# Kernel tuning notes

Hardware: AMD Instinct MI355X
Metric: run time of the kernel (lower is better)

Reference implementation:

```python
import jax, jax.numpy as jnp
import numpy as np

N_HEADS = 16
D_HEAD = 64
N_ROTATE = 32
ROPE_BASE = 10000.0
MAX_LEN = 2048  # round_up_to_multiple_of_256(keep count); static for jit
BATCH, SEQ = 2, 4096


def setup_inputs() -> dict:
    key = jax.random.key(0)
    kq, kk, kv = jax.random.split(key, 3)
    q = jax.random.normal(kq, (BATCH, N_HEADS, MAX_LEN, D_HEAD), jnp.float32)
    k = jax.random.normal(kk, (BATCH, N_HEADS, SEQ, D_HEAD), jnp.float32)
    v = jax.random.normal(kv, (BATCH, N_HEADS, SEQ, D_HEAD), jnp.float32)
    # causal full mask [batch, seq, seq] and full position ids [batch, seq]
    mask_full = jnp.broadcast_to(jnp.tril(jnp.ones((SEQ, SEQ), bool)), (BATCH, SEQ, SEQ))
    pos_full = jnp.broadcast_to(jnp.arange(SEQ, dtype=jnp.int32), (BATCH, SEQ))
    # skip_mask: exactly MAX_LEN kept tokens per row (random positions)
    rng = np.random.default_rng(0)
    sm = np.zeros((BATCH, SEQ), dtype=bool)
    for i in range(BATCH):
        sm[i, rng.permutation(SEQ)[:MAX_LEN]] = True
    return {"q": q, "k": k, "v": v, "mask_full": mask_full,
            "pos_full": pos_full, "skip_mask": jnp.asarray(sm)}


def _rope_rotate(x, pos):
    # x: [b, h, L, n_rotate], pos: [b, L]
    half = N_ROTATE // 2
    inv_freq = 1.0 / (ROPE_BASE ** (jnp.arange(0, N_ROTATE, 2, dtype=jnp.float32) / N_ROTATE))
    freqs = pos.astype(jnp.float32)[..., None] * inv_freq          # [b, L, half]
    emb = jnp.concatenate([freqs, freqs], axis=-1)[:, None]        # [b, 1, L, n_rotate]
    cos, sin = jnp.cos(emb), jnp.sin(emb)
    x1, x2 = x[..., :half], x[..., half:]
    rot = jnp.concatenate([-x2, x1], axis=-1)                      # rotate_half
    return x * cos + rot * sin


def reference(q, k, v, mask_full, pos_full, skip_mask):
    b, S = skip_mask.shape
    lengths = skip_mask.sum(axis=1)
    # vectorized _trim_attention_mask: stable argsort compacts kept indices to the front
    order = jnp.argsort(jnp.where(skip_mask, 0, 1), axis=1, stable=True)
    idx = order[:, :MAX_LEN]                                       # [b, max_len]
    brow = jnp.arange(b)[:, None]
    mask_trim = mask_full[brow, idx]                               # [b, max_len, S]
    pos_trim = pos_full[brow, idx]                                 # [b, max_len]
    valid = jnp.arange(MAX_LEN)[None, :] < lengths[:, None]
    mask_trim = mask_trim & valid[..., None]
    pos_trim = jnp.where(valid, pos_trim, 0)

    # partial RoPE on first n_rotate channels
    rq = _rope_rotate(q[..., :N_ROTATE], pos_trim)
    rk = _rope_rotate(k[..., :N_ROTATE], pos_full)
    q = jnp.concatenate([rq, q[..., N_ROTATE:]], axis=-1)
    k = jnp.concatenate([rk, k[..., N_ROTATE:]], axis=-1)

    # masked SDPA (bool mask broadcast over heads)
    scale = 1.0 / jnp.sqrt(jnp.float32(D_HEAD))
    scores = jnp.einsum('bhqd,bhkd->bhqk', q, k) * scale
    scores = jnp.where(mask_trim[:, None], scores, jnp.finfo(scores.dtype).min)
    attn = jax.nn.softmax(scores, axis=-1)
    return jnp.einsum('bhqk,bhkd->bhqd', attn, v)
```

## Files before the change

kernel.cpp:

```cpp
#include <hip/hip_runtime.h>
#include <math.h>

#define BB 2
#define HH 16
#define QQ 2048
#define SS 4096
#define DD 64
#define NRH 16
#define NQT 32

typedef unsigned short u16;
typedef unsigned int   u32;
typedef short bhalf8 __attribute__((ext_vector_type(8)));
typedef float f32x4  __attribute__((ext_vector_type(4)));

typedef __attribute__((address_space(1))) const u32 gu32;
typedef __attribute__((address_space(3))) u32 lu32;

#if __has_builtin(__builtin_amdgcn_exp2f)
#define EXP2(x) __builtin_amdgcn_exp2f(x)
#else
#define EXP2(x) exp2f(x)
#endif

union Frag16 { uint4 u; bhalf8 v; u16 s[8]; uint2 d[2]; };

__device__ __forceinline__ u16 f2bf(float f) {
  union { float f; u32 u; } c; c.f = f;
  return (u16)((c.u + 0x7FFFu + ((c.u >> 16) & 1u)) >> 16);
}

__device__ __forceinline__ u32 cvt_pk_bf16(float lo, float hi) {
  u32 r;
  asm("v_cvt_pk_bf16_f32 %0, %1, %2" : "=v"(r) : "v"(lo), "v"(hi));
  return r;
}

__device__ __forceinline__ bhalf8 ldfrag(const u16* p) {
  Frag16 f; f.u = *reinterpret_cast<const uint4*>(p); return f.v;
}

__device__ __forceinline__ void rope32(float* x, int pos) {
  const float step = 0.8304820237218405f;
  const float fp = (float)pos;
#pragma unroll
  for (int i = 0; i < NRH; ++i) {
    float ang = fp * exp2f(-step * (float)i);
    float sv, cv;
    __sincosf(ang, &sv, &cv);
    float a = x[i], b = x[i + NRH];
    x[i]       = a * cv - b * sv;
    x[i + NRH] = b * cv + a * sv;
  }
}

__global__ void prep_idx_kernel(const unsigned char* __restrict__ sm,
                                int* __restrict__ idx) {
  __shared__ int wsum[4];
  __shared__ int modes;
  const int tid = threadIdx.x;
  const int b = (int)blockIdx.x;

  int c = 0;
  for (int i = 0; i < 32; ++i) c += (sm[tid * 32 + i] != 0) ? 1 : 0;
#pragma unroll
  for (int off = 32; off; off >>= 1) c += __shfl_down(c, off);
  if ((tid & 63) == 0) wsum[tid >> 6] = c;
  __syncthreads();
  if (tid == 0) modes = (wsum[0] + wsum[1] + wsum[2] + wsum[3] > 3000) ? 1 : 0;
  __syncthreads();
  const bool byteMode = (modes != 0);
  const u32* sm32 = (const u32*)sm;

  const int base = b * SS + tid * 16;
  u32 flags = 0;
  for (int i = 0; i < 16; ++i) {
    bool f = byteMode ? (sm[base + i] != 0) : (sm32[base + i] != 0);
    flags |= ((u32)(f ? 1 : 0)) << i;
  }
  int cnt = __popc(flags);
  int vv = cnt;
#pragma unroll
  for (int off = 1; off < 64; off <<= 1) {
    int t = __shfl_up(vv, off);
    if ((tid & 63) >= off) vv += t;
  }
  __syncthreads();
  if ((tid & 63) == 63) wsum[tid >> 6] = vv;
  __syncthreads();
  int add = 0;
  for (int w2 = 0; w2 < (tid >> 6); ++w2) add += wsum[w2];
  int p = vv - cnt + add;
  for (int i = 0; i < 16; ++i) {
    if (flags & (1u << i)) {
      if (p < QQ) idx[b * QQ + p] = tid * 16 + i;
      ++p;
    }
  }
}

__global__ __launch_bounds__(256) void prep_kv_kernel(const float* __restrict__ k,
                                                      const float* __restrict__ v,
                                                      u16* __restrict__ kbf,
                                                      u16* __restrict__ vt) {
  __shared__ u16 tile[64][72];
  if (blockIdx.x < 512) {
    int r = blockIdx.x * 256 + threadIdx.x;
    int pos = r & (SS - 1);
    float x[64];
    const float4* src = (const float4*)(k + (size_t)r * DD);
#pragma unroll
    for (int i = 0; i < 16; ++i) {
      float4 t = src[i];
      x[4 * i] = t.x; x[4 * i + 1] = t.y; x[4 * i + 2] = t.z; x[4 * i + 3] = t.w;
    }
    rope32(x, pos);
    u16 tmp[64];
#pragma unroll
    for (int i = 0; i < 64; ++i) tmp[i] = f2bf(x[i]);
    uint4* dst = (uint4*)(kbf + (size_t)r * DD);
#pragma unroll
    for (int i = 0; i < 8; ++i) dst[i] = ((uint4*)tmp)[i];
  } else {
    int blk = (int)blockIdx.x - 512;
    int bh = blk >> 6;
    int jt = blk & 63;
    int t = threadIdx.x;
    int jl = t >> 2;
    int dc = (t & 3) * 16;
    const float4* src = (const float4*)(v + ((size_t)(bh * SS + jt * 64 + jl)) * DD + dc);
#pragma unroll
    for (int i = 0; i < 4; ++i) {
      float4 f = src[i];
      tile[jl][dc + 4 * i]     = f2bf(f.x);
      tile[jl][dc + 4 * i + 1] = f2bf(f.y);
      tile[jl][dc + 4 * i + 2] = f2bf(f.z);
      tile[jl][dc + 4 * i + 3] = f2bf(f.w);
    }
    __syncthreads();
    int d = t >> 2;
    int c = t & 3;
    u16 o[16];
#pragma unroll
    for (int m = 0; m < 16; ++m)
      o[m] = tile[4 * c + (m >> 2) + ((m & 3) << 4)][d];
    uint4* dst = (uint4*)(vt + ((size_t)(bh * DD + d)) * SS + jt * 64 + c * 16);
    dst[0] = ((uint4*)o)[0];
    dst[1] = ((uint4*)o)[1];
  }
}

__device__ __forceinline__ void stage_tiles(const char* kb_bh, const char* vt_bh,
                                            u16* Kb, u16* Vb, int t0,
                                            int w, int srow, int schk) {
#pragma unroll
  for (int p2 = 0; p2 < 2; ++p2) {
    const int rr = w * 16 + p2 * 8 + srow;
    {
      const char* g = kb_bh + (size_t)(t0 + rr) * 128 + ((schk ^ (rr & 7)) * 16);
      lu32* l = (lu32*)((char*)Kb + (w * 16 + p2 * 8) * 128);
      __builtin_amdgcn_global_load_lds((gu32*)g, l, 16, 0, 0);
    }
    {
      const char* g = vt_bh + (size_t)rr * (SS * 2) + t0 * 2 + ((schk ^ (rr & 7)) * 16);
      lu32* l = (lu32*)((char*)Vb + (w * 16 + p2 * 8) * 128);
      __builtin_amdgcn_global_load_lds((gu32*)g, l, 16, 0, 0);
    }
  }
}

template <bool MASKED>
__device__ __forceinline__ void attn_tile(
    const u16* __restrict__ Kb, const u16* __restrict__ Vb, u16* __restrict__ pb,
    int t0, int grp, int col,
    int bnd0, int bnd1, int bnd2, int bnd3,
    int paIdx0, int paIdx1,
    int pwIdx0, int pwIdx1, int pwIdx2, int pwIdx3,
    bhalf8 qa0, bhalf8 qa1,
    f32x4& acc0, f32x4& acc1, f32x4& acc2, f32x4& acc3,
    float& l0, float& l1, float& l2, float& l3) {
  const int swz = col & 7;
  f32x4 s0 = {0.f, 0.f, 0.f, 0.f}, s1 = s0, s2 = s0, s3 = s0;
  {
    const u16* kr0 = Kb + (0 * 16 + col) * 64;
    const u16* kr1 = Kb + (1 * 16 + col) * 64;
    const u16* kr2 = Kb + (2 * 16 + col) * 64;
    const u16* kr3 = Kb + (3 * 16 + col) * 64;
    __builtin_amdgcn_s_setprio(1);
    s0 = __builtin_amdgcn_mfma_f32_16x16x32_bf16(qa0, ldfrag(kr0 + ((grp ^ swz) * 8)), s0, 0, 0, 0);
    s1 = __builtin_amdgcn_mfma_f32_16x16x32_bf16(qa0, ldfrag(kr1 + ((grp ^ swz) * 8)), s1, 0, 0, 0);
    s2 = __builtin_amdgcn_mfma_f32_16x16x32_bf16(qa0, ldfrag(kr2 + ((grp ^ swz) * 8)), s2, 0, 0, 0);
    s3 = __builtin_amdgcn_mfma_f32_16x16x32_bf16(qa0, ldfrag(kr3 + ((grp ^ swz) * 8)), s3, 0, 0, 0);
    s0 = __builtin_amdgcn_mfma_f32_16x16x32_bf16(qa1, ldfrag(kr0 + (((4 + grp) ^ swz) * 8)), s0, 0, 0, 0);
    s1 = __builtin_amdgcn_mfma_f32_16x16x32_bf16(qa1, ldfrag(kr1 + (((4 + grp) ^ swz) * 8)), s1, 0, 0, 0);
    s2 = __builtin_amdgcn_mfma_f32_16x16x32_bf16(qa1, ldfrag(kr2 + (((4 + grp) ^ swz) * 8)), s2, 0, 0, 0);
    s3 = __builtin_amdgcn_mfma_f32_16x16x32_bf16(qa1, ldfrag(kr3 + (((4 + grp) ^ swz) * 8)), s3, 0, 0, 0);
    __builtin_amdgcn_s_setprio(0);
  }

  const int key0 = t0 + col;
#define SM_ROW(R, BND, LACC, PWI)                                              \
  {                                                                            \
    float p0, p1, p2v, p3;                                                     \
    if (MASKED) {                                                              \
      p0  = (key0      <= (BND)) ? EXP2(s0[R] - 16.f) : 0.f;                   \
      p1  = (key0 + 16 <= (BND)) ? EXP2(s1[R] - 16.f) : 0.f;                   \
      p2v = (key0 + 32 <= (BND)) ? EXP2(s2[R] - 16.f) : 0.f;                   \
      p3  = (key0 + 48 <= (BND)) ? EXP2(s3[R] - 16.f) : 0.f;                   \
    } else {                                                                   \
      p0  = EXP2(s0[R] - 16.f);                                                \
      p1  = EXP2(s1[R] - 16.f);                                                \
      p2v = EXP2(s2[R] - 16.f);                                                \
      p3  = EXP2(s3[R] - 16.f);                                                \
    }                                                                          \
    (LACC) += (p0 + p1) + (p2v + p3);                                          \
    uint2 pw;                                                                  \
    pw.x = cvt_pk_bf16(p0, p1);                                                \
    pw.y = cvt_pk_bf16(p2v, p3);                                               \
    *(uint2*)(pb + (PWI)) = pw;                                                \
  }
  SM_ROW(0, bnd0, l0, pwIdx0)
  SM_ROW(1, bnd1, l1, pwIdx1)
  SM_ROW(2, bnd2, l2, pwIdx2)
  SM_ROW(3, bnd3, l3, pwIdx3)
#undef SM_ROW

  bhalf8 pa0, pa1;
  {
    Frag16 f0, f1;
    f0.u = *(const uint4*)(pb + paIdx0);
    f1.u = *(const uint4*)(pb + paIdx1);
    pa0 = f0.v; pa1 = f1.v;
  }

  {
    const u16* vr0 = Vb + (0 * 16 + col) * 64;
    const u16* vr1 = Vb + (1 * 16 + col) * 64;
    const u16* vr2 = Vb + (2 * 16 + col) * 64;
    const u16* vr3 = Vb + (3 * 16 + col) * 64;
    __builtin_amdgcn_s_setprio(1);
    acc0 = __builtin_amdgcn_mfma_f32_16x16x32_bf16(pa0, ldfrag(vr0 + ((grp ^ swz) * 8)), acc0, 0, 0, 0);
    acc1 = __builtin_amdgcn_mfma_f32_16x16x32_bf16(pa0, ldfrag(vr1 + ((grp ^ swz) * 8)), acc1, 0, 0, 0);
    acc2 = __builtin_amdgcn_mfma_f32_16x16x32_bf16(pa0, ldfrag(vr2 + ((grp ^ swz) * 8)), acc2, 0, 0, 0);
    acc3 = __builtin_amdgcn_mfma_f32_16x16x32_bf16(pa0, ldfrag(vr3 + ((grp ^ swz) * 8)), acc3, 0, 0, 0);
    acc0 = __builtin_amdgcn_mfma_f32_16x16x32_bf16(pa1, ldfrag(vr0 + (((4 + grp) ^ swz) * 8)), acc0, 0, 0, 0);
    acc1 = __builtin_amdgcn_mfma_f32_16x16x32_bf16(pa1, ldfrag(vr1 + (((4 + grp) ^ swz) * 8)), acc1, 0, 0, 0);
    acc2 = __builtin_amdgcn_mfma_f32_16x16x32_bf16(pa1, ldfrag(vr2 + (((4 + grp) ^ swz) * 8)), acc2, 0, 0, 0);
    acc3 = __builtin_amdgcn_mfma_f32_16x16x32_bf16(pa1, ldfrag(vr3 + (((4 + grp) ^ swz) * 8)), acc3, 0, 0, 0);
    __builtin_amdgcn_s_setprio(0);
  }
}

__global__ __launch_bounds__(256, 4) void attn_mfma_kernel(
    const float* __restrict__ qsrc, const u16* __restrict__ kbf,
    const u16* __restrict__ vt, const int* __restrict__ idx,
    float* __restrict__ out) {
  __shared__ u16 KbufA[64 * 64];
  __shared__ u16 VbufA[64 * 64];
  __shared__ u16 KbufB[64 * 64];
  __shared__ u16 VbufB[64 * 64];
  __shared__ __align__(16) u16 Pbuf[4][16 * 64];

  const int blk = (int)blockIdx.x;
  const int bh  = blk & 31;
  const int qt  = (NQT - 1) - (blk >> 5);
  const int q0  = qt * 64;
  const int b   = bh >> 4;
  const int tid  = threadIdx.x;
  const int w    = tid >> 6;
  const int lane = tid & 63;
  const int grp  = lane >> 4;
  const int col  = lane & 15;

  const char* kb_bh = (const char*)(kbf + (size_t)bh * SS * DD);
  const char* vt_bh = (const char*)(vt + (size_t)bh * DD * SS);

  const int srow = lane >> 3;
  const int schk = lane & 7;

  u16* pb = Pbuf[w];

  const int* idxb = idx + b * QQ + q0;
  const int bnd0 = idxb[w * 16 + grp * 4 + 0];
  const int bnd1 = idxb[w * 16 + grp * 4 + 1];
  const int bnd2 = idxb[w * 16 + grp * 4 + 2];
  const int bnd3 = idxb[w * 16 + grp * 4 + 3];
  const int wave_minb = idxb[w * 16];
  const int wave_maxb = idxb[w * 16 + 15];
  const int maxbound  = idxb[63];
  const int ntiles = (maxbound >> 6) + 1;

  const int paIdx0 = col * 64 + ((grp ^ (col & 7)) << 3);
  const int paIdx1 = col * 64 + (((grp + 4) ^ (col & 7)) << 3);
  const int qg = grp * 4;
  const int pwIdx0 = (qg + 0) * 64 + ((((col >> 1) ^ ((qg + 0) & 7))) << 3) + ((col & 1) << 2);
  const int pwIdx1 = (qg + 1) * 64 + ((((col >> 1) ^ ((qg + 1) & 7))) << 3) + ((col & 1) << 2);
  const int pwIdx2 = (qg + 2) * 64 + ((((col >> 1) ^ ((qg + 2) & 7))) << 3) + ((col & 1) << 2);
  const int pwIdx3 = (qg + 3) * 64 + ((((col >> 1) ^ ((qg + 3) & 7))) << 3) + ((col & 1) << 2);

  bhalf8 qa0, qa1;
  {
    const int qrow = q0 + w * 16 + col;
    const int mypos = idx[b * QQ + qrow];
    const float* qr = qsrc + (size_t)(bh * QQ + qrow) * DD;
    const int lof = (grp & 1) * 8;
    float4 A0 = *(const float4*)(qr + lof);
    float4 A1 = *(const float4*)(qr + lof + 4);
    float4 B0 = *(const float4*)(qr + 16 + lof);
    float4 B1 = *(const float4*)(qr + 16 + lof + 4);
    float4 C0 = *(const float4*)(qr + 32 + grp * 8);
    float4 C1 = *(const float4*)(qr + 32 + grp * 8 + 4);
    float xlo[8] = {A0.x, A0.y, A0.z, A0.w, A1.x, A1.y, A1.z, A1.w};
    float xhi[8] = {B0.x, B0.y, B0.z, B0.w, B1.x, B1.y, B1.z, B1.w};
    float xq1[8] = {C0.x, C0.y, C0.z, C0.w, C1.x, C1.y, C1.z, C1.w};
    const float scq = 0.125f * 1.44269504088896f;
    const float fp = (float)mypos;
    Frag16 f0, f1;
#pragma unroll
    for (int j = 0; j < 8; ++j) {
      float ang = fp * exp2f(-0.8304820237218405f * (float)(lof + j));
      float sv, cv;
      __sincosf(ang, &sv, &cv);
      float val = (grp >= 2) ? (xhi[j] * cv + xlo[j] * sv)
                             : (xlo[j] * cv - xhi[j] * sv);
      f0.s[j] = f2bf(val * scq);
      f1.s[j] = f2bf(xq1[j] * scq);
    }
    qa0 = f0.v; qa1 = f1.v;
  }

  f32x4 acc0 = {0.f, 0.f, 0.f, 0.f}, acc1 = acc0, acc2 = acc0, acc3 = acc0;
  float l0 = 0.f, l1 = 0.f, l2 = 0.f, l3 = 0.f;

  stage_tiles(kb_bh, vt_bh, KbufA, VbufA, 0, w, srow, schk);
  __syncthreads();

  for (int ti = 0; ti < ntiles; ti += 2) {
    const bool has1 = (ti + 1) < ntiles;
    if (has1) stage_tiles(kb_bh, vt_bh, KbufB, VbufB, (ti + 1) << 6, w, srow, schk);
    {
      const int t0 = ti << 6;
      if (t0 <= wave_maxb) {
        if (t0 + 63 <= wave_minb)
          attn_tile<false>(KbufA, VbufA, pb, t0, grp, col, bnd0, bnd1, bnd2, bnd3,
                           paIdx0, paIdx1, pwIdx0, pwIdx1, pwIdx2, pwIdx3,
                           qa0, qa1, acc0, acc1, acc2, acc3, l0, l1, l2, l3);
        else
          attn_tile<true>(KbufA, VbufA, pb, t0, grp, col, bnd0, bnd1, bnd2, bnd3,
                          paIdx0, paIdx1, pwIdx0, pwIdx1, pwIdx2, pwIdx3,
                          qa0, qa1, acc0, acc1, acc2, acc3, l0, l1, l2, l3);
      }
    }
    __syncthreads();
    if (has1) {
      if (ti + 2 < ntiles)
        stage_tiles(kb_bh, vt_bh, KbufA, VbufA, (ti + 2) << 6, w, srow, schk);
      {
        const int t0 = (ti + 1) << 6;
        if (t0 <= wave_maxb) {
          if (t0 + 63 <= wave_minb)
            attn_tile<false>(KbufB, VbufB, pb, t0, grp, col, bnd0, bnd1, bnd2, bnd3,
                             paIdx0, paIdx1, pwIdx0, pwIdx1, pwIdx2, pwIdx3,
                             qa0, qa1, acc0, acc1, acc2, acc3, l0, l1, l2, l3);
          else
            attn_tile<true>(KbufB, VbufB, pb, t0, grp, col, bnd0, bnd1, bnd2, bnd3,
                            paIdx0, paIdx1, pwIdx0, pwIdx1, pwIdx2, pwIdx3,
                            qa0, qa1, acc0, acc1, acc2, acc3, l0, l1, l2, l3);
        }
      }
      __syncthreads();
    }
  }

#pragma unroll
  for (int mdel = 1; mdel < 16; mdel <<= 1) {
    l0 += __shfl_xor(l0, mdel);
    l1 += __shfl_xor(l1, mdel);
    l2 += __shfl_xor(l2, mdel);
    l3 += __shfl_xor(l3, mdel);
  }
  float i0 = 1.f / l0, i1 = 1.f / l1, i2 = 1.f / l2, i3 = 1.f / l3;
  float* ob = out + (size_t)(bh * QQ + q0 + w * 16 + grp * 4) * DD + col;
#pragma unroll
  for (int r = 0; r < 4; ++r) {
    float iv = (r == 0) ? i0 : (r == 1) ? i1 : (r == 2) ? i2 : i3;
    ob[(size_t)r * DD + 0]  = acc0[r] * iv;
    ob[(size_t)r * DD + 16] = acc1[r] * iv;
    ob[(size_t)r * DD + 32] = acc2[r] * iv;
    ob[(size_t)r * DD + 48] = acc3[r] * iv;
  }
}

__global__ __launch_bounds__(64) void attn_fb_kernel(const float* __restrict__ q,
                                                     const float* __restrict__ ksrc,
                                                     const float* __restrict__ v,
                                                     const int* __restrict__ idx,
                                                     float* __restrict__ out) {
  int t = (int)(gridDim.x - 1u - blockIdx.x);
  int sub = t >> 5;
  int bh = t & 31;
  int b = bh >> 4;
  int lane = threadIdx.x;
  int qi = sub * 64 + lane;
  const int bound = idx[b * QQ + qi];

  float qreg[64];
  {
    const float4* qp = (const float4*)(q + ((size_t)bh * QQ + qi) * DD);
#pragma unroll
    for (int i = 0; i < 16; ++i) {
      float4 t4 = qp[i];
      qreg[4 * i] = t4.x; qreg[4 * i + 1] = t4.y;
      qreg[4 * i + 2] = t4.z; qreg[4 * i + 3] = t4.w;
    }
  }
  rope32(qreg, bound);
#pragma unroll
  for (int i = 0; i < 64; ++i) qreg[i] *= 0.125f;

  const float* kbase = ksrc + (size_t)bh * SS * DD;
  const float* vbase = v + (size_t)bh * SS * DD;
  float acc[64];
#pragma unroll
  for (int i = 0; i < 64; ++i) acc[i] = 0.f;
  float mrun = -INFINITY, lrun = 0.f;

  for (int j = 0; j <= bound; ++j) {
    float ka[64];
    const float4* kp = (const float4*)(kbase + (size_t)j * DD);
#pragma unroll
    for (int i = 0; i < 16; ++i) {
      float4 t4 = kp[i];
      ka[4 * i] = t4.x; ka[4 * i + 1] = t4.y;
      ka[4 * i + 2] = t4.z; ka[4 * i + 3] = t4.w;
    }
    rope32(ka, j);
    float s0 = 0.f, s1 = 0.f, s2 = 0.f, s3 = 0.f;
#pragma unroll
    for (int i = 0; i < 16; ++i) {
      s0 = fmaf(qreg[4 * i], ka[4 * i], s0);
      s1 = fmaf(qreg[4 * i + 1], ka[4 * i + 1], s1);
      s2 = fmaf(qreg[4 * i + 2], ka[4 * i + 2], s2);
      s3 = fmaf(qreg[4 * i + 3], ka[4 * i + 3], s3);
    }
    float sc = (s0 + s1) + (s2 + s3);
    if (sc > mrun) {
      float alpha = __expf(mrun - sc);
      lrun *= alpha;
#pragma unroll
      for (int i = 0; i < 64; ++i) acc[i] *= alpha;
      mrun = sc;
    }
    float pw = __expf(sc - mrun);
    lrun += pw;
    const float4* vp = (const float4*)(vbase + (size_t)j * DD);
#pragma unroll
    for (int i = 0; i < 16; ++i) {
      float4 t4 = vp[i];
      acc[4 * i] = fmaf(pw, t4.x, acc[4 * i]);
      acc[4 * i + 1] = fmaf(pw, t4.y, acc[4 * i + 1]);
      acc[4 * i + 2] = fmaf(pw, t4.z, acc[4 * i + 2]);
      acc[4 * i + 3] = fmaf(pw, t4.w, acc[4 * i + 3]);
    }
  }
  float inv = 1.0f / lrun;
  float4* op = (float4*)(out + ((size_t)bh * QQ + qi) * DD);
#pragma unroll
  for (int i = 0; i < 16; ++i) {
    float4 t4;
    t4.x = acc[4 * i] * inv; t4.y = acc[4 * i + 1] * inv;
    t4.z = acc[4 * i + 2] * inv; t4.w = acc[4 * i + 3] * inv;
    op[i] = t4;
  }
}

extern "C" void kernel_launch(void* const* d_in, const int* in_sizes, int n_in,
                              void* d_out, int out_size, void* d_ws, size_t ws_size,
                              hipStream_t stream) {
  (void)in_sizes; (void)n_in; (void)out_size;
  const float* q = (const float*)d_in[0];
  const float* k = (const float*)d_in[1];
  const float* v = (const float*)d_in[2];
  const unsigned char* skip = (const unsigned char*)d_in[5];
  float* out = (float*)d_out;

  char* base = (char*)d_ws;
  int* idx = (int*)base;
  const size_t kbytes = (size_t)BB * HH * SS * DD * 2;
  u16* kbf = (u16*)(base + 16384);
  u16* vtb = (u16*)(base + 16384 + kbytes);
  const size_t need = 16384 + 2 * kbytes;

  prep_idx_kernel<<<2, 256, 0, stream>>>(skip, idx);
  if (ws_size >= need) {
    prep_kv_kernel<<<512 + BB * HH * 64, 256, 0, stream>>>(k, v, kbf, vtb);
    attn_mfma_kernel<<<NQT * 32, 256, 0, stream>>>(q, kbf, vtb, idx, out);
  } else {
    attn_fb_kernel<<<1024, 64, 0, stream>>>(q, k, v, idx, out);
  }
}
```

Measured before the change: 296.8 us.

## Double query rows per wave to reuse K/V fragments across two MFMA row groups

Each wave now handles 32 query rows (two 16-row groups) instead of 16, so the block covers 128 queries and the grid halves. Every K and V LDS fragment load now feeds two MFMAs, halving LDS reads and K/V staging per query. Block order is interleaved (descending then ascending tiles) to balance causal work. The cost is more registers, with the occupancy hint dropped from launch bounds, a larger P buffer, fewer blocks, and an explicit lgkmcnt wait plus sched barrier that may reduce overlap.

```diff
diff --git a/kernel.cpp b/kernel.cpp
--- a/kernel.cpp
+++ b/kernel.cpp
@@ -7,7 +7,7 @@
 #define SS 4096
 #define DD 64
 #define NRH 16
-#define NQT 32
+#define NQT128 16
 
 typedef unsigned short u16;
 typedef unsigned int   u32;
@@ -173,45 +173,67 @@
 __device__ __forceinline__ void attn_tile(
     const u16* __restrict__ Kb, const u16* __restrict__ Vb, u16* __restrict__ pb,
     int t0, int grp, int col,
-    int bnd0, int bnd1, int bnd2, int bnd3,
-    int paIdx0, int paIdx1,
-    int pwIdx0, int pwIdx1, int pwIdx2, int pwIdx3,
-    bhalf8 qa0, bhalf8 qa1,
-    f32x4& acc0, f32x4& acc1, f32x4& acc2, f32x4& acc3,
-    float& l0, float& l1, float& l2, float& l3) {
+    int bndA0, int bndA1, int bndA2, int bndA3,
+    int bndB0, int bndB1, int bndB2, int bndB3,
+    int paA0, int paA1, int paB0, int paB1,
+    int pwA0, int pwA1, int pwA2, int pwA3,
+    int pwB0, int pwB1, int pwB2, int pwB3,
+    bhalf8 qaA0, bhalf8 qaA1, bhalf8 qaB0, bhalf8 qaB1,
+    f32x4& accA0, f32x4& accA1, f32x4& accA2, f32x4& accA3,
+    f32x4& accB0, f32x4& accB1, f32x4& accB2, f32x4& accB3,
+    float& lA0, float& lA1, float& lA2, float& lA3,
+    float& lB0, float& lB1, float& lB2, float& lB3) {
   const int swz = col & 7;
-  f32x4 s0 = {0.f, 0.f, 0.f, 0.f}, s1 = s0, s2 = s0, s3 = s0;
+  f32x4 z = {0.f, 0.f, 0.f, 0.f};
+  f32x4 sA0 = z, sA1 = z, sA2 = z, sA3 = z;
+  f32x4 sB0 = z, sB1 = z, sB2 = z, sB3 = z;
   {
     const u16* kr0 = Kb + (0 * 16 + col) * 64;
     const u16* kr1 = Kb + (1 * 16 + col) * 64;
     const u16* kr2 = Kb + (2 * 16 + col) * 64;
     const u16* kr3 = Kb + (3 * 16 + col) * 64;
     __builtin_amdgcn_s_setprio(1);
-    s0 = __builtin_amdgcn_mfma_f32_16x16x32_bf16(qa0, ldfrag(kr0 + ((grp ^ swz) * 8)), s0, 0, 0, 0);
-    s1 = __builtin_amdgcn_mfma_f32_16x16x32_bf16(qa0, ldfrag(kr1 + ((grp ^ swz) * 8)), s1, 0, 0, 0);
-    s2 = __builtin_amdgcn_mfma_f32_16x16x32_bf16(qa0, ldfrag(kr2 + ((grp ^ swz) * 8)), s2, 0, 0, 0);
-    s3 = __builtin_amdgcn_mfma_f32_16x16x32_bf16(qa0, ldfrag(kr3 + ((grp ^ swz) * 8)), s3, 0, 0, 0);
-    s0 = __builtin_amdgcn_mfma_f32_16x16x32_bf16(qa1, ldfrag(kr0 + (((4 + grp) ^ swz) * 8)), s0, 0, 0, 0);
-    s1 = __builtin_amdgcn_mfma_f32_16x16x32_bf16(qa1, ldfrag(kr1 + (((4 + grp) ^ swz) * 8)), s1, 0, 0, 0);
-    s2 = __builtin_amdgcn_mfma_f32_16x16x32_bf16(qa1, ldfrag(kr2 + (((4 + grp) ^ swz) * 8)), s2, 0, 0, 0);
-    s3 = __builtin_amdgcn_mfma_f32_16x16x32_bf16(qa1, ldfrag(kr3 + (((4 + grp) ^ swz) * 8)), s3, 0, 0, 0);
+    bhalf8 b0 = ldfrag(kr0 + ((grp ^ swz) * 8));
+    sA0 = __builtin_amdgcn_mfma_f32_16x16x32_bf16(qaA0, b0, sA0, 0, 0, 0);
+    sB0 = __builtin_amdgcn_mfma_f32_16x16x32_bf16(qaB0, b0, sB0, 0, 0, 0);
+    bhalf8 b1 = ldfrag(kr1 + ((grp ^ swz) * 8));
+    sA1 = __builtin_amdgcn_mfma_f32_16x16x32_bf16(qaA0, b1, sA1, 0, 0, 0);
+    sB1 = __builtin_amdgcn_mfma_f32_16x16x32_bf16(qaB0, b1, sB1, 0, 0, 0);
+    bhalf8 b2 = ldfrag(kr2 + ((grp ^ swz) * 8));
+    sA2 = __builtin_amdgcn_mfma_f32_16x16x32_bf16(qaA0, b2, sA2, 0, 0, 0);
+    sB2 = __builtin_amdgcn_mfma_f32_16x16x32_bf16(qaB0, b2, sB2, 0, 0, 0);
+    bhalf8 b3 = ldfrag(kr3 + ((grp ^ swz) * 8));
+    sA3 = __builtin_amdgcn_mfma_f32_16x16x32_bf16(qaA0, b3, sA3, 0, 0, 0);
+    sB3 = __builtin_amdgcn_mfma_f32_16x16x32_bf16(qaB0, b3, sB3, 0, 0, 0);
+    bhalf8 c0 = ldfrag(kr0 + (((4 + grp) ^ swz) * 8));
+    sA0 = __builtin_amdgcn_mfma_f32_16x16x32_bf16(qaA1, c0, sA0, 0, 0, 0);
+    sB0 = __builtin_amdgcn_mfma_f32_16x16x32_bf16(qaB1, c0, sB0, 0, 0, 0);
+    bhalf8 c1 = ldfrag(kr1 + (((4 + grp) ^ swz) * 8));
+    sA1 = __builtin_amdgcn_mfma_f32_16x16x32_bf16(qaA1, c1, sA1, 0, 0, 0);
+    sB1 = __builtin_amdgcn_mfma_f32_16x16x32_bf16(qaB1, c1, sB1, 0, 0, 0);
+    bhalf8 c2 = ldfrag(kr2 + (((4 + grp) ^ swz) * 8));
+    sA2 = __builtin_amdgcn_mfma_f32_16x16x32_bf16(qaA1, c2, sA2, 0, 0, 0);
+    sB2 = __builtin_amdgcn_mfma_f32_16x16x32_bf16(qaB1, c2, sB2, 0, 0, 0);
+    bhalf8 c3 = ldfrag(kr3 + (((4 + grp) ^ swz) * 8));
+    sA3 = __builtin_amdgcn_mfma_f32_16x16x32_bf16(qaA1, c3, sA3, 0, 0, 0);
+    sB3 = __builtin_amdgcn_mfma_f32_16x16x32_bf16(qaB1, c3, sB3, 0, 0, 0);
     __builtin_amdgcn_s_setprio(0);
   }
 
   const int key0 = t0 + col;
-#define SM_ROW(R, BND, LACC, PWI)                                              \
+#define SM_ROW(S0, S1, S2, S3, R, BND, LACC, PWI)                              \
   {                                                                            \
     float p0, p1, p2v, p3;                                                     \
     if (MASKED) {                                                              \
-      p0  = (key0      <= (BND)) ? EXP2(s0[R] - 16.f) : 0.f;                   \
-      p1  = (key0 + 16 <= (BND)) ? EXP2(s1[R] - 16.f) : 0.f;                   \
-      p2v = (key0 + 32 <= (BND)) ? EXP2(s2[R] - 16.f) : 0.f;                   \
-      p3  = (key0 + 48 <= (BND)) ? EXP2(s3[R] - 16.f) : 0.f;                   \
+      p0  = (key0      <= (BND)) ? EXP2(S0[R] - 16.f) : 0.f;                   \
+      p1  = (key0 + 16 <= (BND)) ? EXP2(S1[R] - 16.f) : 0.f;                   \
+      p2v = (key0 + 32 <= (BND)) ? EXP2(S2[R] - 16.f) : 0.f;                   \
+      p3  = (key0 + 48 <= (BND)) ? EXP2(S3[R] - 16.f) : 0.f;                   \
     } else {                                                                   \
-      p0  = EXP2(s0[R] - 16.f);                                                \
-      p1  = EXP2(s1[R] - 16.f);                                                \
-      p2v = EXP2(s2[R] - 16.f);                                                \
-      p3  = EXP2(s3[R] - 16.f);                                                \
+      p0  = EXP2(S0[R] - 16.f);                                                \
+      p1  = EXP2(S1[R] - 16.f);                                                \
+      p2v = EXP2(S2[R] - 16.f);                                                \
+      p3  = EXP2(S3[R] - 16.f);                                                \
     }                                                                          \
     (LACC) += (p0 + p1) + (p2v + p3);                                          \
     uint2 pw;                                                                  \
@@ -219,18 +241,27 @@
     pw.y = cvt_pk_bf16(p2v, p3);                                               \
     *(uint2*)(pb + (PWI)) = pw;                                                \
   }
-  SM_ROW(0, bnd0, l0, pwIdx0)
-  SM_ROW(1, bnd1, l1, pwIdx1)
-  SM_ROW(2, bnd2, l2, pwIdx2)
-  SM_ROW(3, bnd3, l3, pwIdx3)
+  SM_ROW(sA0, sA1, sA2, sA3, 0, bndA0, lA0, pwA0)
+  SM_ROW(sA0, sA1, sA2, sA3, 1, bndA1, lA1, pwA1)
+  SM_ROW(sA0, sA1, sA2, sA3, 2, bndA2, lA2, pwA2)
+  SM_ROW(sA0, sA1, sA2, sA3, 3, bndA3, lA3, pwA3)
+  SM_ROW(sB0, sB1, sB2, sB3, 0, bndB0, lB0, pwB0)
+  SM_ROW(sB0, sB1, sB2, sB3, 1, bndB1, lB1, pwB1)
+  SM_ROW(sB0, sB1, sB2, sB3, 2, bndB2, lB2, pwB2)
+  SM_ROW(sB0, sB1, sB2, sB3, 3, bndB3, lB3, pwB3)
 #undef SM_ROW
 
-  bhalf8 pa0, pa1;
-  {
-    Frag16 f0, f1;
-    f0.u = *(const uint4*)(pb + paIdx0);
-    f1.u = *(const uint4*)(pb + paIdx1);
-    pa0 = f0.v; pa1 = f1.v;
+  asm volatile("s_waitcnt lgkmcnt(0)" ::: "memory");
+  __builtin_amdgcn_sched_barrier(0);
+
+  bhalf8 paA_0, paA_1, paB_0, paB_1;
+  {
+    Frag16 f0, f1, g0, g1;
+    f0.u = *(const uint4*)(pb + paA0);
+    f1.u = *(const uint4*)(pb + paA1);
+    g0.u = *(const uint4*)(pb + paB0);
+    g1.u = *(const uint4*)(pb + paB1);
+    paA_0 = f0.v; paA_1 = f1.v; paB_0 = g0.v; paB_1 = g1.v;
   }
 
   {
@@ -239,19 +270,35 @@
     const u16* vr2 = Vb + (2 * 16 + col) * 64;
     const u16* vr3 = Vb + (3 * 16 + col) * 64;
     __builtin_amdgcn_s_setprio(1);
-    acc0 = __builtin_amdgcn_mfma_f32_16x16x32_bf16(pa0, ldfrag(vr0 + ((grp ^ swz) * 8)), acc0, 0, 0, 0);
-    acc1 = __builtin_amdgcn_mfma_f32_16x16x32_bf16(pa0, ldfrag(vr1 + ((grp ^ swz) * 8)), acc1, 0, 0, 0);
-    acc2 = __builtin_amdgcn_mfma_f32_16x16x32_bf16(pa0, ldfrag(vr2 + ((grp ^ swz) * 8)), acc2, 0, 0, 0);
-    acc3 = __builtin_amdgcn_mfma_f32_16x16x32_bf16(pa0, ldfrag(vr3 + ((grp ^ swz) * 8)), acc3, 0, 0, 0);
-    acc0 = __builtin_amdgcn_mfma_f32_16x16x32_bf16(pa1, ldfrag(vr0 + (((4 + grp) ^ swz) * 8)), acc0, 0, 0, 0);
-    acc1 = __builtin_amdgcn_mfma_f32_16x16x32_bf16(pa1, ldfrag(vr1 + (((4 + grp) ^ swz) * 8)), acc1, 0, 0, 0);
-    acc2 = __builtin_amdgcn_mfma_f32_16x16x32_bf16(pa1, ldfrag(vr2 + (((4 + grp) ^ swz) * 8)), acc2, 0, 0, 0);
-    acc3 = __builtin_amdgcn_mfma_f32_16x16x32_bf16(pa1, ldfrag(vr3 + (((4 + grp) ^ swz) * 8)), acc3, 0, 0, 0);
+    bhalf8 v0 = ldfrag(vr0 + ((grp ^ swz) * 8));
+    accA0 = __builtin_amdgcn_mfma_f32_16x16x32_bf16(paA_0, v0, accA0, 0, 0, 0);
+    accB0 = __builtin_amdgcn_mfma_f32_16x16x32_bf16(paB_0, v0, accB0, 0, 0, 0);
+    bhalf8 v1 = ldfrag(vr1 + ((grp ^ swz) * 8));
+    accA1 = __builtin_amdgcn_mfma_f32_16x16x32_bf16(paA_0, v1, accA1, 0, 0, 0);
+    accB1 = __builtin_amdgcn_mfma_f32_16x16x32_bf16(paB_0, v1, accB1, 0, 0, 0);
+    bhalf8 v2 = ldfrag(vr2 + ((grp ^ swz) * 8));
+    accA2 = __builtin_amdgcn_mfma_f32_16x16x32_bf16(paA_0, v2, accA2, 0, 0, 0);
+    accB2 = __builtin_amdgcn_mfma_f32_16x16x32_bf16(paB_0, v2, accB2, 0, 0, 0);
+    bhalf8 v3 = ldfrag(vr3 + ((grp ^ swz) * 8));
+    accA3 = __builtin_amdgcn_mfma_f32_16x16x32_bf16(paA_0, v3, accA3, 0, 0, 0);
+    accB3 = __builtin_amdgcn_mfma_f32_16x16x32_bf16(paB_0, v3, accB3, 0, 0, 0);
+    bhalf8 u0 = ldfrag(vr0 + (((4 + grp) ^ swz) * 8));
+    accA0 = __builtin_amdgcn_mfma_f32_16x16x32_bf16(paA_1, u0, accA0, 0, 0, 0);
+    accB0 = __builtin_amdgcn_mfma_f32_16x16x32_bf16(paB_1, u0, accB0, 0, 0, 0);
+    bhalf8 u1 = ldfrag(vr1 + (((4 + grp) ^ swz) * 8));
+    accA1 = __builtin_amdgcn_mfma_f32_16x16x32_bf16(paA_1, u1, accA1, 0, 0, 0);
+    accB1 = __builtin_amdgcn_mfma_f32_16x16x32_bf16(paB_1, u1, accB1, 0, 0, 0);
+    bhalf8 u2 = ldfrag(vr2 + (((4 + grp) ^ swz) * 8));
+    accA2 = __builtin_amdgcn_mfma_f32_16x16x32_bf16(paA_1, u2, accA2, 0, 0, 0);
+    accB2 = __builtin_amdgcn_mfma_f32_16x16x32_bf16(paB_1, u2, accB2, 0, 0, 0);
+    bhalf8 u3 = ldfrag(vr3 + (((4 + grp) ^ swz) * 8));
+    accA3 = __builtin_amdgcn_mfma_f32_16x16x32_bf16(paA_1, u3, accA3, 0, 0, 0);
+    accB3 = __builtin_amdgcn_mfma_f32_16x16x32_bf16(paB_1, u3, accB3, 0, 0, 0);
     __builtin_amdgcn_s_setprio(0);
   }
 }
 
-__global__ __launch_bounds__(256, 4) void attn_mfma_kernel(
+__global__ __launch_bounds__(256) void attn_mfma_kernel(
     const float* __restrict__ qsrc, const u16* __restrict__ kbf,
     const u16* __restrict__ vt, const int* __restrict__ idx,
     float* __restrict__ out) {
@@ -259,12 +306,13 @@
   __shared__ u16 VbufA[64 * 64];
   __shared__ u16 KbufB[64 * 64];
   __shared__ u16 VbufB[64 * 64];
-  __shared__ __align__(16) u16 Pbuf[4][16 * 64];
+  __shared__ __align__(16) u16 Pbuf[4][32 * 64];
 
   const int blk = (int)blockIdx.x;
   const int bh  = blk & 31;
-  const int qt  = (NQT - 1) - (blk >> 5);
-  const int q0  = qt * 64;
+  const int rank = blk >> 5;
+  const int qt  = (rank < 8) ? (15 - 2 * rank) : (2 * (rank - 8));
+  const int q0  = qt * 128;
   const int b   = bh >> 4;
   const int tid  = threadIdx.x;
   const int w    = tid >> 6;
@@ -281,26 +329,36 @@
   u16* pb = Pbuf[w];
 
   const int* idxb = idx + b * QQ + q0;
-  const int bnd0 = idxb[w * 16 + grp * 4 + 0];
-  const int bnd1 = idxb[w * 16 + grp * 4 + 1];
-  const int bnd2 = idxb[w * 16 + grp * 4 + 2];
-  const int bnd3 = idxb[w * 16 + grp * 4 + 3];
-  const int wave_minb = idxb[w * 16];
-  const int wave_maxb = idxb[w * 16 + 15];
-  const int maxbound  = idxb[63];
+  const int bndA0 = idxb[w * 32 + grp * 4 + 0];
+  const int bndA1 = idxb[w * 32 + grp * 4 + 1];
+  const int bndA2 = idxb[w * 32 + grp * 4 + 2];
+  const int bndA3 = idxb[w * 32 + grp * 4 + 3];
+  const int bndB0 = idxb[w * 32 + 16 + grp * 4 + 0];
+  const int bndB1 = idxb[w * 32 + 16 + grp * 4 + 1];
+  const int bndB2 = idxb[w * 32 + 16 + grp * 4 + 2];
+  const int bndB3 = idxb[w * 32 + 16 + grp * 4 + 3];
+  const int wave_minb = idxb[w * 32];
+  const int wave_maxb = idxb[w * 32 + 31];
+  const int maxbound  = idxb[127];
   const int ntiles = (maxbound >> 6) + 1;
 
-  const int paIdx0 = col * 64 + ((grp ^ (col & 7)) << 3);
-  const int paIdx1 = col * 64 + (((grp + 4) ^ (col & 7)) << 3);
+  const int paA0 = col * 64 + ((grp ^ (col & 7)) << 3);
+  const int paA1 = col * 64 + (((grp + 4) ^ (col & 7)) << 3);
+  const int paB0 = (16 + col) * 64 + ((grp ^ (col & 7)) << 3);
+  const int paB1 = (16 + col) * 64 + (((grp + 4) ^ (col & 7)) << 3);
   const int qg = grp * 4;
-  const int pwIdx0 = (qg + 0) * 64 + ((((col >> 1) ^ ((qg + 0) & 7))) << 3) + ((col & 1) << 2);
-  const int pwIdx1 = (qg + 1) * 64 + ((((col >> 1) ^ ((qg + 1) & 7))) << 3) + ((col & 1) << 2);
-  const int pwIdx2 = (qg + 2) * 64 + ((((col >> 1) ^ ((qg + 2) & 7))) << 3) + ((col & 1) << 2);
-  const int pwIdx3 = (qg + 3) * 64 + ((((col >> 1) ^ ((qg + 3) & 7))) << 3) + ((col & 1) << 2);
-
-  bhalf8 qa0, qa1;
-  {
-    const int qrow = q0 + w * 16 + col;
+  const int pwA0 = (qg + 0) * 64 + ((((col >> 1) ^ ((qg + 0) & 7))) << 3) + ((col & 1) << 2);
+  const int pwA1 = (qg + 1) * 64 + ((((col >> 1) ^ ((qg + 1) & 7))) << 3) + ((col & 1) << 2);
+  const int pwA2 = (qg + 2) * 64 + ((((col >> 1) ^ ((qg + 2) & 7))) << 3) + ((col & 1) << 2);
+  const int pwA3 = (qg + 3) * 64 + ((((col >> 1) ^ ((qg + 3) & 7))) << 3) + ((col & 1) << 2);
+  const int pwB0 = (16 + qg + 0) * 64 + ((((col >> 1) ^ ((qg + 0) & 7))) << 3) + ((col & 1) << 2);
+  const int pwB1 = (16 + qg + 1) * 64 + ((((col >> 1) ^ ((qg + 1) & 7))) << 3) + ((col & 1) << 2);
+  const int pwB2 = (16 + qg + 2) * 64 + ((((col >> 1) ^ ((qg + 2) & 7))) << 3) + ((col & 1) << 2);
+  const int pwB3 = (16 + qg + 3) * 64 + ((((col >> 1) ^ ((qg + 3) & 7))) << 3) + ((col & 1) << 2);
+
+  bhalf8 qaA0, qaA1, qaB0, qaB1;
+  {
+    const int qrow = q0 + w * 32 + col;
     const int mypos = idx[b * QQ + qrow];
     const float* qr = qsrc + (size_t)(bh * QQ + qrow) * DD;
     const int lof = (grp & 1) * 8;
@@ -326,11 +384,52 @@
       f0.s[j] = f2bf(val * scq);
       f1.s[j] = f2bf(xq1[j] * scq);
     }
-    qa0 = f0.v; qa1 = f1.v;
-  }
-
-  f32x4 acc0 = {0.f, 0.f, 0.f, 0.f}, acc1 = acc0, acc2 = acc0, acc3 = acc0;
-  float l0 = 0.f, l1 = 0.f, l2 = 0.f, l3 = 0.f;
+    qaA0 = f0.v; qaA1 = f1.v;
+  }
+  {
+    const int qrow = q0 + w * 32 + 16 + col;
+    const int mypos = idx[b * QQ + qrow];
+    const float* qr = qsrc + (size_t)(bh * QQ + qrow) * DD;
+    const int lof = (grp & 1) * 8;
+    float4 A0 = *(const float4*)(qr + lof);
+    float4 A1 = *(const float4*)(qr + lof + 4);
+    float4 B0 = *(const float4*)(qr + 16 + lof);
+    float4 B1 = *(const float4*)(qr + 16 + lof + 4);
+    float4 C0 = *(const float4*)(qr + 32 + grp * 8);
+    float4 C1 = *(const float4*)(qr + 32 + grp * 8 + 4);
+    float xlo[8] = {A0.x, A0.y, A0.z, A0.w, A1.x, A1.y, A1.z, A1.w};
+    float xhi[8] = {B0.x, B0.y, B0.z, B0.w, B1.x, B1.y, B1.z, B1.w};
+    float xq1[8] = {C0.x, C0.y, C0.z, C0.w, C1.x, C1.y, C1.z, C1.w};
+    const float scq = 0.125f * 1.44269504088896f;
+    const float fp = (float)mypos;
+    Frag16 f0, f1;
+#pragma unroll
+    for (int j = 0; j < 8; ++j) {
+      float ang = fp * exp2f(-0.8304820237218405f * (float)(lof + j));
+      float sv, cv;
+      __sincosf(ang, &sv, &cv);
+      float val = (grp >= 2) ? (xhi[j] * cv + xlo[j] * sv)
+                             : (xlo[j] * cv - xhi[j] * sv);
+      f0.s[j] = f2bf(val * scq);
+      f1.s[j] = f2bf(xq1[j] * scq);
+    }
+    qaB0 = f0.v; qaB1 = f1.v;
+  }
+
+  f32x4 z = {0.f, 0.f, 0.f, 0.f};
+  f32x4 accA0 = z, accA1 = z, accA2 = z, accA3 = z;
+  f32x4 accB0 = z, accB1 = z, accB2 = z, accB3 = z;
+  float lA0 = 0.f, lA1 = 0.f, lA2 = 0.f, lA3 = 0.f;
+  float lB0 = 0.f, lB1 = 0.f, lB2 = 0.f, lB3 = 0.f;
+
+#define ATTN_CALL(M, KB, VB, T0)                                               \
+  attn_tile<M>(KB, VB, pb, T0, grp, col,                                       \
+               bndA0, bndA1, bndA2, bndA3, bndB0, bndB1, bndB2, bndB3,         \
+               paA0, paA1, paB0, paB1,                                         \
+               pwA0, pwA1, pwA2, pwA3, pwB0, pwB1, pwB2, pwB3,                 \
+               qaA0, qaA1, qaB0, qaB1,                                         \
+               accA0, accA1, accA2, accA3, accB0, accB1, accB2, accB3,         \
+               lA0, lA1, lA2, lA3, lB0, lB1, lB2, lB3)
 
   stage_tiles(kb_bh, vt_bh, KbufA, VbufA, 0, w, srow, schk);
   __syncthreads();
@@ -341,14 +440,8 @@
     {
       const int t0 = ti << 6;
       if (t0 <= wave_maxb) {
-        if (t0 + 63 <= wave_minb)
-          attn_tile<false>(KbufA, VbufA, pb, t0, grp, col, bnd0, bnd1, bnd2, bnd3,
-                           paIdx0, paIdx1, pwIdx0, pwIdx1, pwIdx2, pwIdx3,
-                           qa0, qa1, acc0, acc1, acc2, acc3, l0, l1, l2, l3);
-        else
-          attn_tile<true>(KbufA, VbufA, pb, t0, grp, col, bnd0, bnd1, bnd2, bnd3,
-                          paIdx0, paIdx1, pwIdx0, pwIdx1, pwIdx2, pwIdx3,
-                          qa0, qa1, acc0, acc1, acc2, acc3, l0, l1, l2, l3);
+        if (t0 + 63 <= wave_minb) ATTN_CALL(false, KbufA, VbufA, t0);
+        else                      ATTN_CALL(true,  KbufA, VbufA, t0);
       }
     }
     __syncthreads();
@@ -358,36 +451,49 @@
       {
         const int t0 = (ti + 1) << 6;
         if (t0 <= wave_maxb) {
-          if (t0 + 63 <= wave_minb)
-            attn_tile<false>(KbufB, VbufB, pb, t0, grp, col, bnd0, bnd1, bnd2, bnd3,
-                             paIdx0, paIdx1, pwIdx0, pwIdx1, pwIdx2, pwIdx3,
-                             qa0, qa1, acc0, acc1, acc2, acc3, l0, l1, l2, l3);
-          else
-            attn_tile<true>(KbufB, VbufB, pb, t0, grp, col, bnd0, bnd1, bnd2, bnd3,
-                            paIdx0, paIdx1, pwIdx0, pwIdx1, pwIdx2, pwIdx3,
-                            qa0, qa1, acc0, acc1, acc2, acc3, l0, l1, l2, l3);
+          if (t0 + 63 <= wave_minb) ATTN_CALL(false, KbufB, VbufB, t0);
+          else                      ATTN_CALL(true,  KbufB, VbufB, t0);
         }
       }
       __syncthreads();
     }
   }
+#undef ATTN_CALL
 
 #pragma unroll
   for (int mdel = 1; mdel < 16; mdel <<= 1) {
-    l0 += __shfl_xor(l0, mdel);
-    l1 += __shfl_xor(l1, mdel);
-    l2 += __shfl_xor(l2, mdel);
-    l3 += __shfl_xor(l3, mdel);
-  }
-  float i0 = 1.f / l0, i1 = 1.f / l1, i2 = 1.f / l2, i3 = 1.f / l3;
-  float* ob = out + (size_t)(bh * QQ + q0 + w * 16 + grp * 4) * DD + col;
-#pragma unroll
-  for (int r = 0; r < 4; ++r) {
-    float iv = (r == 0) ? i0 : (r == 1) ? i1 : (r == 2) ? i2 : i3;
-    ob[(size_t)r * DD + 0]  = acc0[r] * iv;
-    ob[(size_t)r * DD + 16] = acc1[r] * iv;
-    ob[(size_t)r * DD + 32] = acc2[r] * iv;
-    ob[(size_t)r * DD + 48] = acc3[r] * iv;
+    lA0 += __shfl_xor(lA0, mdel);
+    lA1 += __shfl_xor(lA1, mdel);
+    lA2 += __shfl_xor(lA2, mdel);
+    lA3 += __shfl_xor(lA3, mdel);
+    lB0 += __shfl_xor(lB0, mdel);
+    lB1 += __shfl_xor(lB1, mdel);
+    lB2 += __shfl_xor(lB2, mdel);
+    lB3 += __shfl_xor(lB3, mdel);
+  }
+  {
+    float i0 = 1.f / lA0, i1 = 1.f / lA1, i2 = 1.f / lA2, i3 = 1.f / lA3;
+    float* ob = out + (size_t)(bh * QQ + q0 + w * 32 + grp * 4) * DD + col;
+#pragma unroll
+    for (int r = 0; r < 4; ++r) {
+      float iv = (r == 0) ? i0 : (r == 1) ? i1 : (r == 2) ? i2 : i3;
+      ob[(size_t)r * DD + 0]  = accA0[r] * iv;
+      ob[(size_t)r * DD + 16] = accA1[r] * iv;
+      ob[(size_t)r * DD + 32] = accA2[r] * iv;
+      ob[(size_t)r * DD + 48] = accA3[r] * iv;
+    }
+  }
+  {
+    float i0 = 1.f / lB0, i1 = 1.f / lB1, i2 = 1.f / lB2, i3 = 1.f / lB3;
+    float* ob = out + (size_t)(bh * QQ + q0 + w * 32 + 16 + grp * 4) * DD + col;
+#pragma unroll
+    for (int r = 0; r < 4; ++r) {
+      float iv = (r == 0) ? i0 : (r == 1) ? i1 : (r == 2) ? i2 : i3;
+      ob[(size_t)r * DD + 0]  = accB0[r] * iv;
+      ob[(size_t)r * DD + 16] = accB1[r] * iv;
+      ob[(size_t)r * DD + 32] = accB2[r] * iv;
+      ob[(size_t)r * DD + 48] = accB3[r] * iv;
+    }
   }
 }
 
@@ -494,7 +600,7 @@
   prep_idx_kernel<<<2, 256, 0, stream>>>(skip, idx);
   if (ws_size >= need) {
     prep_kv_kernel<<<512 + BB * HH * 64, 256, 0, stream>>>(k, v, kbf, vtb);
-    attn_mfma_kernel<<<NQT * 32, 256, 0, stream>>>(q, kbf, vtb, idx, out);
+    attn_mfma_kernel<<<NQT128 * 32, 256, 0, stream>>>(q, kbf, vtb, idx, out);
   } else {
     attn_fb_kernel<<<1024, 64, 0, stream>>>(q, k, v, idx, out);
   }
```

New measurement: 305.0 us. 2.8% more time.
